# Optimization experiments

Measured on AMD Instinct MI355X. Metric: run time of the kernel, lower is better.

Reference implementation:

```python
import jax, jax.numpy as jnp
import numpy as np

N_NODES = 100000
N_EDGES = 1000000
DIM = 64
BN_EPS = 1e-5


def setup_inputs() -> dict:
    key = jax.random.key(0)
    k_x, k_src, k_off, k_w, k_b = jax.random.split(key, 5)
    x = jax.random.normal(k_x, (N_NODES, DIM), dtype=jnp.float32)
    # Build edges with src != dst so add_remaining_self_loops semantics reduce to
    # appending one self-loop per node (no pre-existing self loops).
    src = jax.random.randint(k_src, (N_EDGES,), 0, N_NODES, dtype=jnp.int64)
    off = jax.random.randint(k_off, (N_EDGES,), 1, N_NODES, dtype=jnp.int64)
    dst = (src + off) % N_NODES
    edge_index = jnp.stack([src, dst], axis=0)
    lin_w = jax.random.normal(k_w, (DIM, DIM), dtype=jnp.float32) * (1.0 / np.sqrt(DIM))
    lin_b = jax.random.normal(k_b, (DIM,), dtype=jnp.float32) * 0.01
    bn_gamma = jnp.ones((DIM,), dtype=jnp.float32)
    bn_beta = jnp.zeros((DIM,), dtype=jnp.float32)
    return {"x": x, "edge_index": edge_index, "lin_w": lin_w, "lin_b": lin_b,
            "bn_gamma": bn_gamma, "bn_beta": bn_beta}


def reference(x, edge_index, lin_w, lin_b, bn_gamma, bn_beta):
    N = x.shape[0]
    loops = jnp.arange(N, dtype=edge_index.dtype)
    src = jnp.concatenate([edge_index[0], loops])  # add_remaining_self_loops
    dst = jnp.concatenate([edge_index[1], loops])
    # edge_weight is rebound to None inside MySAGEConv.forward, so message == x_j
    msgs = jnp.take(x, src, axis=0)                      # [E+N, D] gather
    summed = jax.ops.segment_sum(msgs, dst, num_segments=N)
    deg = jax.ops.segment_sum(jnp.ones_like(dst, dtype=x.dtype), dst, num_segments=N)
    aggr = summed / deg[:, None]                         # scatter-mean (deg >= 1)
    out = aggr @ lin_w.T + lin_b                         # linear
    # BatchNorm1d, training mode (batch stats, biased variance)
    mean = out.mean(axis=0)
    var = out.var(axis=0)
    out = (out - mean) * jax.lax.rsqrt(var + BN_EPS) * bn_gamma + bn_beta
    out = out + x                                        # residual (in_dim == out_dim)
    return jax.nn.relu(out)
```

## Files before the change

kernel.cpp:

```cpp
#include <hip/hip_runtime.h>

#define N_NODES 100000
#define N_EDGES 1000000
#define DIM 64
#define BN_EPS 1e-5f

#define CAP 40
#define SEG_SHIFT 10
#define SEG_NODES 1024
#define NSEG 98
#define SEGCAP 11264
#define BCAP 96
#define EPB 4096
#define NBIN1 245
#define CONV_BLOCKS 3125
#define OVF_CAP 4096
#define GATHER_BLOCKS (N_NODES / 32)

typedef __attribute__((ext_vector_type(8))) short short8_t;
typedef __attribute__((ext_vector_type(4))) float f32x4;

__device__ inline unsigned bf16rne(float f) {
    unsigned u = __float_as_uint(f);
    return (u + 0x7FFFu + ((u >> 16) & 1u)) >> 16;
}
__device__ inline unsigned pack2(float a, float b) {
    return bf16rne(a) | (bf16rne(b) << 16);
}
__device__ inline void unp_add(unsigned d, float& e0, float& e1) {
    e0 += __uint_as_float(d << 16);
    e1 += __uint_as_float(d & 0xFFFF0000u);
}
__device__ inline void add8(float* acc, uint4 v) {
    unp_add(v.x, acc[0], acc[1]);
    unp_add(v.y, acc[2], acc[3]);
    unp_add(v.z, acc[4], acc[5]);
    unp_add(v.w, acc[6], acc[7]);
}

__global__ __launch_bounds__(256) void k_bin1(const int* __restrict__ ei,
                                              const float4* __restrict__ x4,
                                              const float* __restrict__ W,
                                              unsigned* __restrict__ seg_buf,
                                              int* __restrict__ seg_cnt,
                                              int* __restrict__ ovf_cnt,
                                              uint2* __restrict__ ovf,
                                              uint4* __restrict__ xh,
                                              unsigned short* __restrict__ Wb) {
    __shared__ int cnt[NSEG];
    __shared__ int base[NSEG];
    __shared__ unsigned pairs[NSEG][BCAP];

    int b = blockIdx.x;
    if (b == NBIN1 + CONV_BLOCKS) {
        for (int t = threadIdx.x; t < DIM * DIM / 2; t += 256) {
            float2 w2 = ((const float2*)W)[t];
            ((unsigned*)Wb)[t] = pack2(w2.x, w2.y);
        }
        return;
    }
    if (b >= NBIN1) {
        int g = (b - NBIN1) * 256 + threadIdx.x;
        float4 lo = x4[2 * g];
        float4 hi = x4[2 * g + 1];
        uint4 r;
        r.x = pack2(lo.x, lo.y);
        r.y = pack2(lo.z, lo.w);
        r.z = pack2(hi.x, hi.y);
        r.w = pack2(hi.z, hi.w);
        xh[8 + g] = r;
        return;
    }

    for (int t = threadIdx.x; t < NSEG; t += 256) cnt[t] = 0;
    __syncthreads();

    const int base4 = b * (EPB / 4);
#pragma unroll
    for (int k = 0; k < 4; ++k) {
        int i4 = base4 + k * 256 + threadIdx.x;
        if (i4 < N_EDGES / 4) {
            int4 s4 = ((const int4*)ei)[i4];
            int4 d4 = ((const int4*)(ei + N_EDGES))[i4];
            int ss[4] = {s4.x, s4.y, s4.z, s4.w};
            int dd[4] = {d4.x, d4.y, d4.z, d4.w};
#pragma unroll
            for (int q = 0; q < 4; ++q) {
                int seg = (unsigned)dd[q] >> SEG_SHIFT;
                unsigned pk = ((unsigned)(dd[q] & (SEG_NODES - 1)) << 17)
                            | (unsigned)ss[q];
                int p = atomicAdd(&cnt[seg], 1);
                if (p < BCAP) {
                    pairs[seg][p] = pk;
                } else {
                    int g = atomicAdd(ovf_cnt, 1);
                    if (g < OVF_CAP) ovf[g] = make_uint2((unsigned)ss[q], (unsigned)dd[q]);
                }
            }
        }
    }
    __syncthreads();

    if (threadIdx.x < NSEG) {
        int c = min(cnt[threadIdx.x], BCAP);
        base[threadIdx.x] = atomicAdd(&seg_cnt[threadIdx.x], c);
    }
    __syncthreads();

    const int wave = threadIdx.x >> 6, lane = threadIdx.x & 63;
    for (int seg = wave; seg < NSEG; seg += 4) {
        int c = min(cnt[seg], BCAP);
        int bs = base[seg];
        for (int i = lane; i < c; i += 64) {
            int pos = bs + i;
            if (pos < SEGCAP) seg_buf[seg * SEGCAP + pos] = pairs[seg][i];
        }
    }
}

struct ScanS { int lcnt[32]; unsigned lists[32][CAP]; };
struct MmS { unsigned short ab[32 * 72]; float red0[4][32]; float red1[4][32]; };
union GatherU { ScanS sc; MmS mm; };

__global__ __launch_bounds__(256) void k_gather_linear(
        const uint4* __restrict__ xh,
        const unsigned* __restrict__ seg_buf,
        const int* __restrict__ seg_cnt,
        const int* __restrict__ ovf_cnt,
        const uint2* __restrict__ ovf,
        const unsigned short* __restrict__ Wb,
        const float* __restrict__ bias,
        float* __restrict__ lin_out,
        float* __restrict__ stats8) {
    __shared__ GatherU sh;
    const int lane = threadIdx.x & 63;
    const int wave = threadIdx.x >> 6;
    const int seg = blockIdx.x >> 5;
    const int winbase = (blockIdx.x & 31) * 32;

    if (threadIdx.x < 32) sh.sc.lcnt[threadIdx.x] = 0;
    __syncthreads();

    int n = seg_cnt[seg];
    if (n > SEGCAP) n = SEGCAP;
    const unsigned* sb = seg_buf + seg * SEGCAP;

    auto proc = [&](unsigned p) {
        int wloc = (int)(p >> 17) - winbase;
        if ((unsigned)wloc < 32u) {
            int pos = atomicAdd(&sh.sc.lcnt[wloc], 1);
            if (pos < CAP) sh.sc.lists[wloc][pos] = p & 0x1FFFFu;
        }
    };

    for (int i = threadIdx.x * 4; i < n; i += 1024) {
        uint4 p4;
        if (i + 4 <= n) {
            p4 = *(const uint4*)(sb + i);
        } else {
            p4.x = sb[i];
            p4.y = (i + 1 < n) ? sb[i + 1] : 0xFFFFFFFFu;
            p4.z = (i + 2 < n) ? sb[i + 2] : 0xFFFFFFFFu;
            p4.w = 0xFFFFFFFFu;
        }
        proc(p4.x); proc(p4.y); proc(p4.z); proc(p4.w);
    }
    int oc = *ovf_cnt;
    if (oc > OVF_CAP) oc = OVF_CAP;
    for (int t = threadIdx.x; t < oc; t += 256) {
        uint2 pr = ovf[t];
        if ((int)(pr.y >> SEG_SHIFT) == seg) {
            int wloc = (int)(pr.y & (SEG_NODES - 1)) - winbase;
            if ((unsigned)wloc < 32u) {
                int pos = atomicAdd(&sh.sc.lcnt[wloc], 1);
                if (pos < CAP) sh.sc.lists[wloc][pos] = pr.x;
            }
        }
    }
    __syncthreads();

    const int sub = lane >> 3, f8 = lane & 7;
    const int r = wave * 8 + sub;
    const int row = blockIdx.x * 32 + r;
    float acc[8] = {0.f, 0.f, 0.f, 0.f, 0.f, 0.f, 0.f, 0.f};
    add8(acc, xh[(row + 1) * 8 + f8]);

    const int ctrue = sh.sc.lcnt[r];
    const int c = (ctrue < CAP) ? ctrue : CAP;
    const int* sp = (const int*)&sh.sc.lists[r][0];
    for (int i = 0; i < c; i += 4) {
        int4 e = *(const int4*)(sp + i);
        int e1 = (i + 1 < c) ? e.y : -1;
        int e2 = (i + 2 < c) ? e.z : -1;
        int e3 = (i + 3 < c) ? e.w : -1;
        uint4 v0 = xh[(e.x + 1) * 8 + f8];
        uint4 v1 = xh[(e1 + 1) * 8 + f8];
        uint4 v2 = xh[(e2 + 1) * 8 + f8];
        uint4 v3 = xh[(e3 + 1) * 8 + f8];
        add8(acc, v0);
        add8(acc, v1);
        add8(acc, v2);
        add8(acc, v3);
    }

    const float inv = 1.0f / (float)(ctrue + 1);
#pragma unroll
    for (int k = 0; k < 8; ++k) acc[k] *= inv;

    __syncthreads();

    uint4 pk;
    pk.x = pack2(acc[0], acc[1]);
    pk.y = pack2(acc[2], acc[3]);
    pk.z = pack2(acc[4], acc[5]);
    pk.w = pack2(acc[6], acc[7]);
    *(uint4*)&sh.mm.ab[(wave * 8 + sub) * 72 + f8 * 8] = pk;
    __syncthreads();

    const int mh = wave & 1, nh = wave >> 1;
    const int m = lane & 15, quad = lane >> 4;

    const unsigned short* ap = &sh.mm.ab[(mh * 16 + m) * 72 + quad * 8];
    short8_t a0 = *(const short8_t*)ap;
    short8_t a1 = *(const short8_t*)(ap + 32);

    const unsigned short* bp0 = Wb + (nh * 32 + m) * 64 + quad * 8;
    short8_t b00 = *(const short8_t*)bp0;
    short8_t b01 = *(const short8_t*)(bp0 + 32);
    const unsigned short* bp1 = bp0 + 16 * 64;
    short8_t b10 = *(const short8_t*)bp1;
    short8_t b11 = *(const short8_t*)(bp1 + 32);

    f32x4 c0 = {0.f, 0.f, 0.f, 0.f}, c1 = {0.f, 0.f, 0.f, 0.f};
    c0 = __builtin_amdgcn_mfma_f32_16x16x32_bf16(a0, b00, c0, 0, 0, 0);
    c0 = __builtin_amdgcn_mfma_f32_16x16x32_bf16(a1, b01, c0, 0, 0, 0);
    c1 = __builtin_amdgcn_mfma_f32_16x16x32_bf16(a0, b10, c1, 0, 0, 0);
    c1 = __builtin_amdgcn_mfma_f32_16x16x32_bf16(a1, b11, c1, 0, 0, 0);

    const int rb = blockIdx.x * 32 + mh * 16 + quad * 4;
#pragma unroll
    for (int f = 0; f < 2; ++f) {
        f32x4 cc = f ? c1 : c0;
        int col = nh * 32 + f * 16 + m;
        float bj = bias[col];
        float q0 = 0.f, q1 = 0.f;
#pragma unroll
        for (int rr = 0; rr < 4; ++rr) {
            float v = cc[rr] + bj;
            lin_out[(rb + rr) * DIM + col] = v;
            q0 += v;
            q1 += v * v;
        }
        q0 += __shfl_xor(q0, 16); q0 += __shfl_xor(q0, 32);
        q1 += __shfl_xor(q1, 16); q1 += __shfl_xor(q1, 32);
        if (quad == 0) {
            sh.mm.red0[wave][f * 16 + m] = q0;
            sh.mm.red1[wave][f * 16 + m] = q1;
        }
    }
    __syncthreads();
    if (threadIdx.x < DIM) {
        int j = threadIdx.x, jh = j >> 5, jl = j & 31;
        float t0 = sh.mm.red0[2 * jh][jl] + sh.mm.red0[2 * jh + 1][jl];
        float t1 = sh.mm.red1[2 * jh][jl] + sh.mm.red1[2 * jh + 1][jl];
        float* sbk = stats8 + (blockIdx.x & 7) * 128;
        atomicAdd(&sbk[j], t0);
        atomicAdd(&sbk[DIM + j], t1);
    }
}

__global__ __launch_bounds__(256) void k_final(const float4* lin4,
                                               const unsigned short* __restrict__ xh16,
                                               const float* __restrict__ stats8,
                                               const float* __restrict__ gamma,
                                               const float* __restrict__ beta,
                                               float4* out4) {
    __shared__ float ss[2][DIM];
    if (threadIdx.x < DIM) {
        int j = threadIdx.x;
        float s0 = 0.f, s1 = 0.f;
#pragma unroll
        for (int b = 0; b < 8; ++b) {
            s0 += stats8[b * 128 + j];
            s1 += stats8[b * 128 + DIM + j];
        }
        const float invN = 1.0f / (float)N_NODES;
        float mean = s0 * invN;
        float var = s1 * invN - mean * mean;
        float scale = gamma[j] * rsqrtf(var + BN_EPS);
        ss[0][j] = scale;
        ss[1][j] = beta[j] - mean * scale;
    }
    __syncthreads();
    int tid = blockIdx.x * blockDim.x + threadIdx.x;
    int row = tid >> 4;
    int j4 = (tid & 15) * 4;
    float4 l = lin4[tid];
    ushort2 h01 = *(const ushort2*)&xh16[(row + 1) * 64 + j4];
    ushort2 h23 = *(const ushort2*)&xh16[(row + 1) * 64 + j4 + 2];
    float4 o;
    o.x = fmaxf(fmaf(l.x, ss[0][j4 + 0], ss[1][j4 + 0])
                + __uint_as_float((unsigned)h01.x << 16), 0.f);
    o.y = fmaxf(fmaf(l.y, ss[0][j4 + 1], ss[1][j4 + 1])
                + __uint_as_float((unsigned)h01.y << 16), 0.f);
    o.z = fmaxf(fmaf(l.z, ss[0][j4 + 2], ss[1][j4 + 2])
                + __uint_as_float((unsigned)h23.x << 16), 0.f);
    o.w = fmaxf(fmaf(l.w, ss[0][j4 + 3], ss[1][j4 + 3])
                + __uint_as_float((unsigned)h23.y << 16), 0.f);
    out4[tid] = o;
}

extern "C" void kernel_launch(void* const* d_in, const int* in_sizes, int n_in,
                              void* d_out, int out_size, void* d_ws, size_t ws_size,
                              hipStream_t stream) {
    const float* x     = (const float*)d_in[0];
    const int*   ei    = (const int*)d_in[1];
    const float* W     = (const float*)d_in[2];
    const float* bias  = (const float*)d_in[3];
    const float* gamma = (const float*)d_in[4];
    const float* beta  = (const float*)d_in[5];
    float* out = (float*)d_out;

    char* ws = (char*)d_ws;
    float*          stats8  = (float*)(ws);
    int*            seg_cnt = (int*)(ws + 4096);
    int*            ovf_cnt = (int*)(ws + 4608);
    uint2*          ovf     = (uint2*)(ws + 4736);
    uint4*          xh      = (uint4*)(ws + 37504);
    unsigned short* Wb      = (unsigned short*)(ws + 12837632);
    unsigned*       seg_buf = (unsigned*)(ws + 12845824);

    hipMemsetAsync(ws, 0, 37632, stream);

    k_bin1<<<NBIN1 + CONV_BLOCKS + 1, 256, 0, stream>>>(
        ei, (const float4*)x, W, seg_buf, seg_cnt, ovf_cnt, ovf, xh, Wb);

    k_gather_linear<<<GATHER_BLOCKS, 256, 0, stream>>>(
        xh, seg_buf, seg_cnt, ovf_cnt, ovf, Wb, bias, out, stats8);

    k_final<<<N_NODES * (DIM / 4) / 256, 256, 0, stream>>>(
        (const float4*)out, (const unsigned short*)xh, stats8, gamma, beta,
        (float4*)out);
}
```

Baseline: 145.2 us.

## Process 128-node windows per gather block to cut segment rescans

```diff
diff --git a/kernel.cpp b/kernel.cpp
--- a/kernel.cpp
+++ b/kernel.cpp
@@ -15,7 +15,8 @@
 #define NBIN1 245
 #define CONV_BLOCKS 3125
 #define OVF_CAP 4096
-#define GATHER_BLOCKS (N_NODES / 32)
+#define WIN 128
+#define GATHER_BLOCKS 784
 
 typedef __attribute__((ext_vector_type(8))) short short8_t;
 typedef __attribute__((ext_vector_type(4))) float f32x4;
@@ -118,10 +119,6 @@
     }
 }
 
-struct ScanS { int lcnt[32]; unsigned lists[32][CAP]; };
-struct MmS { unsigned short ab[32 * 72]; float red0[4][32]; float red1[4][32]; };
-union GatherU { ScanS sc; MmS mm; };
-
 __global__ __launch_bounds__(256) void k_gather_linear(
         const uint4* __restrict__ xh,
         const unsigned* __restrict__ seg_buf,
@@ -132,13 +129,18 @@
         const float* __restrict__ bias,
         float* __restrict__ lin_out,
         float* __restrict__ stats8) {
-    __shared__ GatherU sh;
+    __shared__ int lcnt[WIN];
+    __shared__ __align__(16) unsigned lists[WIN][CAP];
+    __shared__ __align__(16) unsigned short ab[WIN * 72];
+    __shared__ float red0[4][32];
+    __shared__ float red1[4][32];
+
     const int lane = threadIdx.x & 63;
     const int wave = threadIdx.x >> 6;
-    const int seg = blockIdx.x >> 5;
-    const int winbase = (blockIdx.x & 31) * 32;
-
-    if (threadIdx.x < 32) sh.sc.lcnt[threadIdx.x] = 0;
+    const int seg = blockIdx.x >> 3;
+    const int winbase = (blockIdx.x & 7) * WIN;
+
+    for (int t = threadIdx.x; t < WIN; t += 256) lcnt[t] = 0;
     __syncthreads();
 
     int n = seg_cnt[seg];
@@ -147,9 +149,9 @@
 
     auto proc = [&](unsigned p) {
         int wloc = (int)(p >> 17) - winbase;
-        if ((unsigned)wloc < 32u) {
-            int pos = atomicAdd(&sh.sc.lcnt[wloc], 1);
-            if (pos < CAP) sh.sc.lists[wloc][pos] = p & 0x1FFFFu;
+        if ((unsigned)wloc < (unsigned)WIN) {
+            int pos = atomicAdd(&lcnt[wloc], 1);
+            if (pos < CAP) lists[wloc][pos] = p & 0x1FFFFu;
         }
     };
 
@@ -171,58 +173,55 @@
         uint2 pr = ovf[t];
         if ((int)(pr.y >> SEG_SHIFT) == seg) {
             int wloc = (int)(pr.y & (SEG_NODES - 1)) - winbase;
-            if ((unsigned)wloc < 32u) {
-                int pos = atomicAdd(&sh.sc.lcnt[wloc], 1);
-                if (pos < CAP) sh.sc.lists[wloc][pos] = pr.x;
+            if ((unsigned)wloc < (unsigned)WIN) {
+                int pos = atomicAdd(&lcnt[wloc], 1);
+                if (pos < CAP) lists[wloc][pos] = pr.x;
             }
         }
     }
     __syncthreads();
 
     const int sub = lane >> 3, f8 = lane & 7;
-    const int r = wave * 8 + sub;
-    const int row = blockIdx.x * 32 + r;
-    float acc[8] = {0.f, 0.f, 0.f, 0.f, 0.f, 0.f, 0.f, 0.f};
-    add8(acc, xh[(row + 1) * 8 + f8]);
-
-    const int ctrue = sh.sc.lcnt[r];
-    const int c = (ctrue < CAP) ? ctrue : CAP;
-    const int* sp = (const int*)&sh.sc.lists[r][0];
-    for (int i = 0; i < c; i += 4) {
-        int4 e = *(const int4*)(sp + i);
-        int e1 = (i + 1 < c) ? e.y : -1;
-        int e2 = (i + 2 < c) ? e.z : -1;
-        int e3 = (i + 3 < c) ? e.w : -1;
-        uint4 v0 = xh[(e.x + 1) * 8 + f8];
-        uint4 v1 = xh[(e1 + 1) * 8 + f8];
-        uint4 v2 = xh[(e2 + 1) * 8 + f8];
-        uint4 v3 = xh[(e3 + 1) * 8 + f8];
-        add8(acc, v0);
-        add8(acc, v1);
-        add8(acc, v2);
-        add8(acc, v3);
-    }
-
-    const float inv = 1.0f / (float)(ctrue + 1);
-#pragma unroll
-    for (int k = 0; k < 8; ++k) acc[k] *= inv;
-
-    __syncthreads();
-
-    uint4 pk;
-    pk.x = pack2(acc[0], acc[1]);
-    pk.y = pack2(acc[2], acc[3]);
-    pk.z = pack2(acc[4], acc[5]);
-    pk.w = pack2(acc[6], acc[7]);
-    *(uint4*)&sh.mm.ab[(wave * 8 + sub) * 72 + f8 * 8] = pk;
+#pragma unroll
+    for (int s = 0; s < 4; ++s) {
+        const int r = s * 32 + wave * 8 + sub;
+        const int row = blockIdx.x * WIN + r;
+        float acc[8] = {0.f, 0.f, 0.f, 0.f, 0.f, 0.f, 0.f, 0.f};
+        if (row < N_NODES) add8(acc, xh[(row + 1) * 8 + f8]);
+
+        const int ctrue = lcnt[r];
+        const int c = (ctrue < CAP) ? ctrue : CAP;
+        const int* sp = (const int*)&lists[r][0];
+        for (int i = 0; i < c; i += 4) {
+            int4 e = *(const int4*)(sp + i);
+            int e1 = (i + 1 < c) ? e.y : -1;
+            int e2 = (i + 2 < c) ? e.z : -1;
+            int e3 = (i + 3 < c) ? e.w : -1;
+            uint4 v0 = xh[(e.x + 1) * 8 + f8];
+            uint4 v1 = xh[(e1 + 1) * 8 + f8];
+            uint4 v2 = xh[(e2 + 1) * 8 + f8];
+            uint4 v3 = xh[(e3 + 1) * 8 + f8];
+            add8(acc, v0);
+            add8(acc, v1);
+            add8(acc, v2);
+            add8(acc, v3);
+        }
+
+        const float inv = 1.0f / (float)(ctrue + 1);
+#pragma unroll
+        for (int k = 0; k < 8; ++k) acc[k] *= inv;
+
+        uint4 pk;
+        pk.x = pack2(acc[0], acc[1]);
+        pk.y = pack2(acc[2], acc[3]);
+        pk.z = pack2(acc[4], acc[5]);
+        pk.w = pack2(acc[6], acc[7]);
+        *(uint4*)&ab[r * 72 + f8 * 8] = pk;
+    }
     __syncthreads();
 
     const int mh = wave & 1, nh = wave >> 1;
     const int m = lane & 15, quad = lane >> 4;
-
-    const unsigned short* ap = &sh.mm.ab[(mh * 16 + m) * 72 + quad * 8];
-    short8_t a0 = *(const short8_t*)ap;
-    short8_t a1 = *(const short8_t*)(ap + 32);
 
     const unsigned short* bp0 = Wb + (nh * 32 + m) * 64 + quad * 8;
     short8_t b00 = *(const short8_t*)bp0;
@@ -230,42 +229,59 @@
     const unsigned short* bp1 = bp0 + 16 * 64;
     short8_t b10 = *(const short8_t*)bp1;
     short8_t b11 = *(const short8_t*)(bp1 + 32);
-
-    f32x4 c0 = {0.f, 0.f, 0.f, 0.f}, c1 = {0.f, 0.f, 0.f, 0.f};
-    c0 = __builtin_amdgcn_mfma_f32_16x16x32_bf16(a0, b00, c0, 0, 0, 0);
-    c0 = __builtin_amdgcn_mfma_f32_16x16x32_bf16(a1, b01, c0, 0, 0, 0);
-    c1 = __builtin_amdgcn_mfma_f32_16x16x32_bf16(a0, b10, c1, 0, 0, 0);
-    c1 = __builtin_amdgcn_mfma_f32_16x16x32_bf16(a1, b11, c1, 0, 0, 0);
-
-    const int rb = blockIdx.x * 32 + mh * 16 + quad * 4;
-#pragma unroll
-    for (int f = 0; f < 2; ++f) {
-        f32x4 cc = f ? c1 : c0;
-        int col = nh * 32 + f * 16 + m;
-        float bj = bias[col];
-        float q0 = 0.f, q1 = 0.f;
-#pragma unroll
-        for (int rr = 0; rr < 4; ++rr) {
-            float v = cc[rr] + bj;
-            lin_out[(rb + rr) * DIM + col] = v;
-            q0 += v;
-            q1 += v * v;
-        }
-        q0 += __shfl_xor(q0, 16); q0 += __shfl_xor(q0, 32);
-        q1 += __shfl_xor(q1, 16); q1 += __shfl_xor(q1, 32);
-        if (quad == 0) {
-            sh.mm.red0[wave][f * 16 + m] = q0;
-            sh.mm.red1[wave][f * 16 + m] = q1;
-        }
-    }
-    __syncthreads();
+    const float bj0 = bias[nh * 32 + m];
+    const float bj1 = bias[nh * 32 + 16 + m];
+
+    float t0acc = 0.f, t1acc = 0.f;
+
+#pragma unroll
+    for (int s = 0; s < 4; ++s) {
+        const unsigned short* ap = &ab[(s * 32 + mh * 16 + m) * 72 + quad * 8];
+        short8_t a0 = *(const short8_t*)ap;
+        short8_t a1 = *(const short8_t*)(ap + 32);
+
+        f32x4 c0 = {0.f, 0.f, 0.f, 0.f}, c1 = {0.f, 0.f, 0.f, 0.f};
+        c0 = __builtin_amdgcn_mfma_f32_16x16x32_bf16(a0, b00, c0, 0, 0, 0);
+        c0 = __builtin_amdgcn_mfma_f32_16x16x32_bf16(a1, b01, c0, 0, 0, 0);
+        c1 = __builtin_amdgcn_mfma_f32_16x16x32_bf16(a0, b10, c1, 0, 0, 0);
+        c1 = __builtin_amdgcn_mfma_f32_16x16x32_bf16(a1, b11, c1, 0, 0, 0);
+
+        const int rb = blockIdx.x * WIN + s * 32 + mh * 16 + quad * 4;
+#pragma unroll
+        for (int f = 0; f < 2; ++f) {
+            f32x4 cc = f ? c1 : c0;
+            int col = nh * 32 + f * 16 + m;
+            float bj = f ? bj1 : bj0;
+            float q0 = 0.f, q1 = 0.f;
+#pragma unroll
+            for (int rr = 0; rr < 4; ++rr) {
+                float v = cc[rr] + bj;
+                if (rb + rr < N_NODES) {
+                    lin_out[(rb + rr) * DIM + col] = v;
+                    q0 += v;
+                    q1 += v * v;
+                }
+            }
+            q0 += __shfl_xor(q0, 16); q0 += __shfl_xor(q0, 32);
+            q1 += __shfl_xor(q1, 16); q1 += __shfl_xor(q1, 32);
+            if (quad == 0) {
+                red0[wave][f * 16 + m] = q0;
+                red1[wave][f * 16 + m] = q1;
+            }
+        }
+        __syncthreads();
+        if (threadIdx.x < DIM) {
+            int j = threadIdx.x, jh = j >> 5, jl = j & 31;
+            t0acc += red0[2 * jh][jl] + red0[2 * jh + 1][jl];
+            t1acc += red1[2 * jh][jl] + red1[2 * jh + 1][jl];
+        }
+        __syncthreads();
+    }
+
     if (threadIdx.x < DIM) {
-        int j = threadIdx.x, jh = j >> 5, jl = j & 31;
-        float t0 = sh.mm.red0[2 * jh][jl] + sh.mm.red0[2 * jh + 1][jl];
-        float t1 = sh.mm.red1[2 * jh][jl] + sh.mm.red1[2 * jh + 1][jl];
         float* sbk = stats8 + (blockIdx.x & 7) * 128;
-        atomicAdd(&sbk[j], t0);
-        atomicAdd(&sbk[DIM + j], t1);
+        atomicAdd(&sbk[threadIdx.x], t0acc);
+        atomicAdd(&sbk[DIM + threadIdx.x], t1acc);
     }
 }
 
```

Result: no change. 143.1 us (-1.5%).
